# Performance work log

Measured on AMD Instinct MI355X. Metric: run time of the kernel, lower is better.

The kernel has to match this reference:

```python
import jax, jax.numpy as jnp
import numpy as np

N_ITER = 10
N_PRIMAL = 5
N_IONS = 1
B, H, W, A = 1, 96, 96, 60
D = H  # detector bins == H, forced by the reshape in the original code


def _conv(x, w, b):
    y = jax.lax.conv_general_dilated(x, w, (1, 1), [(1, 1), (1, 1)],
                                     dimension_numbers=('NCHW', 'OIHW', 'NCHW'))
    return y + b[None, :, None, None]


def _prelu(x, a):
    return jnp.where(x >= 0, x, a * x)


def _block(x, w1, b1, a1, w2, b2, a2, w3, b3):
    x = _prelu(_conv(x, w1, b1), a1)
    x = _prelu(_conv(x, w2, b2), a2)
    return _conv(x, w3, b3)


def setup_inputs():
    key = jax.random.key(0)
    ks = jax.random.split(key, 12)
    s = 0.05
    dc = 3 * N_IONS      # DualNet input channels
    pc = N_PRIMAL + 1    # PrimalNet input channels
    inp = {
        'dual': jax.random.normal(ks[0], (B, N_IONS, A, D), jnp.float32),
        'primal': jax.random.normal(ks[1], (B, N_PRIMAL, H, W, 1), jnp.float32),
        'g': jax.random.normal(ks[2], (B, N_IONS, A, D), jnp.float32),
        'sysm_angles': jax.random.normal(ks[3], (B, A, H * W, N_IONS * D), jnp.float32) * s,
        'sysm_angles_norm': jax.random.normal(ks[4], (B, A, N_IONS * H, H * W), jnp.float32) * s,
        'dual_w1': jax.random.normal(ks[5], (N_ITER, 32, dc, 3, 3), jnp.float32) * s,
        'dual_b1': jnp.zeros((N_ITER, 32), jnp.float32),
        'dual_a1': jnp.full((N_ITER,), 0.25, jnp.float32),
        'dual_w2': jax.random.normal(ks[6], (N_ITER, 32, 32, 3, 3), jnp.float32) * s,
        'dual_b2': jnp.zeros((N_ITER, 32), jnp.float32),
        'dual_a2': jnp.full((N_ITER,), 0.25, jnp.float32),
        'dual_w3': jax.random.normal(ks[7], (N_ITER, N_IONS, 32, 3, 3), jnp.float32) * s,
        'dual_b3': jnp.zeros((N_ITER, N_IONS), jnp.float32),
        'primal_w1': jax.random.normal(ks[8], (N_ITER, 32, pc, 3, 3), jnp.float32) * s,
        'primal_b1': jnp.zeros((N_ITER, 32), jnp.float32),
        'primal_a1': jnp.full((N_ITER,), 0.25, jnp.float32),
        'primal_w2': jax.random.normal(ks[9], (N_ITER, 32, 32, 3, 3), jnp.float32) * s,
        'primal_b2': jnp.zeros((N_ITER, 32), jnp.float32),
        'primal_a2': jnp.full((N_ITER,), 0.25, jnp.float32),
        'primal_w3': jax.random.normal(ks[10], (N_ITER, N_PRIMAL, 32, 3, 3), jnp.float32) * s,
        'primal_b3': jnp.zeros((N_ITER, N_PRIMAL), jnp.float32),
        'return_all': 0,
    }
    return inp


def _forward(dual, primal, g, sysm_angles, sysm_angles_norm,
             dw1, db1, da1, dw2, db2, da2, dw3, db3,
             pw1, pb1, pa1, pw2, pb2, pa2, pw3, pb3):
    for k in range(N_ITER):
        # forward projection: fortran-flatten primal channel 1 (index h + H*w), batched over all angles
        img_f = primal[:, 1, :, :, 0].transpose(0, 2, 1).reshape(B, H * W)   # [B, H*W]
        prod = jnp.einsum('bamn,bn->bam', sysm_angles_norm, img_f)           # [B, A, N_IONS*H]
        evalop1 = prod.reshape(B, A, H, N_IONS).transpose(0, 3, 1, 2)        # [B, N_IONS, A, D]
        x = jnp.concatenate([dual, evalop1, g], axis=1)
        dual = dual + _block(x, dw1[k], db1[k], da1[k], dw2[k], db2[k], da2[k], dw3[k], db3[k])
        # adjoint (back-projection) summed over angles
        dual2 = dual.transpose(0, 2, 3, 1).reshape(B, A, D * N_IONS)         # [B, A, D*N_IONS]
        vec = jnp.einsum('bavn,ban->bv', sysm_angles, dual2)                 # [B, H*W]
        evalop2 = vec.reshape(B, W, H).transpose(0, 2, 1)[:, None]           # [B, 1, H, W] fortran unflatten
        p2d = primal[..., 0]                                                 # [B, N_PRIMAL, H, W]
        xp = jnp.concatenate([p2d, evalop2], axis=1)
        p2d = p2d + _block(xp, pw1[k], pb1[k], pa1[k], pw2[k], pb2[k], pa2[k], pw3[k], pb3[k])
        primal = p2d[..., None]
    return primal[:, 0:1]  # [B, 1, H, W, 1]


def reference(dual, primal, g, sysm_angles, sysm_angles_norm,
              dual_w1, dual_b1, dual_a1, dual_w2, dual_b2, dual_a2, dual_w3, dual_b3,
              primal_w1, primal_b1, primal_a1, primal_w2, primal_b2, primal_a2, primal_w3, primal_b3,
              return_all):
    return _forward(dual, primal, g, sysm_angles, sysm_angles_norm,
                    dual_w1, dual_b1, dual_a1, dual_w2, dual_b2, dual_a2, dual_w3, dual_b3,
                    primal_w1, primal_b1, primal_a1, primal_w2, primal_b2, primal_a2, primal_w3, primal_b3)
```

## Files before the change

kernel.cpp:

```cpp
#include <hip/hip_runtime.h>

#define AA 60
#define HH 96
#define WW 96
#define DD 96
#define HWP (HH * WW)
#define ADP (AA * DD)
#define NITER 10
#define MATEL (60 * 96 * 9216)

typedef unsigned short ushort8 __attribute__((ext_vector_type(8)));
typedef float float4v __attribute__((ext_vector_type(4)));

__device__ inline float b2f(unsigned short u) {
    return __uint_as_float(((unsigned)u) << 16);
}
__device__ inline unsigned short f2b(float f) {
    unsigned u = __float_as_uint(f);
    u += 0x7FFFu + ((u >> 16) & 1u);
    return (unsigned short)(u >> 16);
}

__global__ __launch_bounds__(256) void cvt_kernel(const float* __restrict__ a,
                                                  const float* __restrict__ b,
                                                  ushort8* __restrict__ da,
                                                  ushort8* __restrict__ db, int n8) {
    int stride = gridDim.x * 256;
    for (int i = blockIdx.x * 256 + threadIdx.x; i < 2 * n8; i += stride) {
        const float* src; ushort8* dst; int j;
        if (i < n8) { src = a; dst = da; j = i; }
        else        { src = b; dst = db; j = i - n8; }
        const float4v* s = reinterpret_cast<const float4v*>(src) + 2 * (size_t)j;
        float4v x = __builtin_nontemporal_load(s);
        float4v y = __builtin_nontemporal_load(s + 1);
        ushort8 o;
        o[0] = f2b(x[0]); o[1] = f2b(x[1]); o[2] = f2b(x[2]); o[3] = f2b(x[3]);
        o[4] = f2b(y[0]); o[5] = f2b(y[1]); o[6] = f2b(y[2]); o[7] = f2b(y[3]);
        dst[j] = o;
    }
}

__global__ __launch_bounds__(256) void init_kernel(const float* __restrict__ dual,
                            const float* __restrict__ g,
                            const float* __restrict__ primal,
                            float* __restrict__ xd, float* __restrict__ xp,
                            float* __restrict__ imgf, float* __restrict__ xp5) {
    int i = blockIdx.x * 256 + threadIdx.x;
    if (i < ADP) { xd[i] = dual[i]; xd[2 * ADP + i] = g[i]; }
    if (i < 5 * HWP) xp[i] = primal[i];
    if (i < HWP) {
        imgf[(i % WW) * HH + i / WW] = primal[HWP + i];
        xp5[i] = 0.f;
    }
}

__global__ __launch_bounds__(256) void einsum1_kernel(const unsigned short* __restrict__ norm,
                               const float* __restrict__ imgf,
                               float* __restrict__ out) {
    int row  = blockIdx.x * 4 + (threadIdx.x >> 6);
    int lane = threadIdx.x & 63;
    const unsigned short* mr = norm + (size_t)row * HWP;
    float s = 0.f;
    for (int k = 0; k < HWP / 512; ++k) {
        int n = 8 * lane + 512 * k;
        ushort8 m8 = *reinterpret_cast<const ushort8*>(mr + n);
        float4 i0 = *reinterpret_cast<const float4*>(imgf + n);
        float4 i1 = *reinterpret_cast<const float4*>(imgf + n + 4);
        s += b2f(m8[0]) * i0.x + b2f(m8[1]) * i0.y + b2f(m8[2]) * i0.z + b2f(m8[3]) * i0.w
           + b2f(m8[4]) * i1.x + b2f(m8[5]) * i1.y + b2f(m8[6]) * i1.z + b2f(m8[7]) * i1.w;
    }
#pragma unroll
    for (int off = 32; off > 0; off >>= 1) s += __shfl_down(s, off);
    if (lane == 0) out[row] = s;
}

__global__ __launch_bounds__(256) void einsum2_kernel(const unsigned short* __restrict__ sysm,
                               const float* __restrict__ xd,
                               float* __restrict__ xp5) {
    __shared__ float sd[4 * DD];
    int t  = threadIdx.x;
    int a0 = (blockIdx.x % 15) * 4;
    int v  = (blockIdx.x / 15) * 256 + t;
    for (int j = t; j < 4 * DD; j += 256) sd[j] = xd[a0 * DD + j];
    __syncthreads();
    float s = 0.f;
    for (int ai = 0; ai < 4; ++ai) {
        const unsigned short* row = sysm + ((size_t)(a0 + ai) * HWP + v) * DD;
        const float* dl = sd + ai * DD;
#pragma unroll
        for (int jj = 0; jj < DD / 8; ++jj) {
            ushort8 m8 = *reinterpret_cast<const ushort8*>(row + 8 * jj);
            s += b2f(m8[0]) * dl[8 * jj]     + b2f(m8[1]) * dl[8 * jj + 1]
               + b2f(m8[2]) * dl[8 * jj + 2] + b2f(m8[3]) * dl[8 * jj + 3]
               + b2f(m8[4]) * dl[8 * jj + 4] + b2f(m8[5]) * dl[8 * jj + 5]
               + b2f(m8[6]) * dl[8 * jj + 6] + b2f(m8[7]) * dl[8 * jj + 7];
        }
    }
    atomicAdd(xp5 + (v % HH) * WW + (v / HH), s);
}

template <int CIN, int NOUT>
__global__ __launch_bounds__(64) void conv_mid(
        const float* __restrict__ in,
        const float* __restrict__ wgt,
        const float* __restrict__ bias,
        const float* __restrict__ alpha,
        float* __restrict__ out,
        int Hc, int Wc) {
    int hw  = Hc * Wc;
    int pix = blockIdx.x * 64 + threadIdx.x;
    int y = pix / Wc, x = pix % Wc;
    int oc0 = blockIdx.y * NOUT;
    const float* wb = wgt + (size_t)oc0 * CIN * 9;
    float a = alpha[0];
    float acc[NOUT];
#pragma unroll
    for (int o = 0; o < NOUT; ++o) acc[o] = bias[oc0 + o];
    for (int ci = 0; ci < CIN; ++ci) {
        const float* ip = in + ci * hw;
#pragma unroll
        for (int ky = 0; ky < 3; ++ky) {
            int yy = y + ky - 1;
            bool yok = (unsigned)yy < (unsigned)Hc;
#pragma unroll
            for (int kx = 0; kx < 3; ++kx) {
                int xx = x + kx - 1;
                bool vok = yok && ((unsigned)xx < (unsigned)Wc);
                float v = ip[vok ? yy * Wc + xx : 0];
                v = vok ? v : 0.f;
#pragma unroll
                for (int o = 0; o < NOUT; ++o)
                    acc[o] += wb[(o * CIN + ci) * 9 + ky * 3 + kx] * v;
            }
        }
    }
#pragma unroll
    for (int o = 0; o < NOUT; ++o) {
        float r = acc[o];
        r = (r >= 0.f) ? r : a * r;
        out[(oc0 + o) * hw + pix] = r;
    }
}

__global__ __launch_bounds__(64) void conv3d_last(const float* __restrict__ in,
        const float* __restrict__ wgt,
        const float* __restrict__ bias,
        float* __restrict__ xd) {
    int pix = blockIdx.x * 64 + threadIdx.x;
    int y = pix / DD, x = pix % DD;
    int c0 = blockIdx.y * 4;
    float r = (blockIdx.y == 0) ? bias[0] : 0.f;
    for (int ci = c0; ci < c0 + 4; ++ci) {
        const float* ip = in + ci * ADP;
#pragma unroll
        for (int ky = 0; ky < 3; ++ky) {
            int yy = y + ky - 1;
            bool yok = (unsigned)yy < (unsigned)AA;
#pragma unroll
            for (int kx = 0; kx < 3; ++kx) {
                int xx = x + kx - 1;
                bool vok = yok && ((unsigned)xx < (unsigned)DD);
                float v = ip[vok ? yy * DD + xx : 0];
                v = vok ? v : 0.f;
                r += wgt[ci * 9 + ky * 3 + kx] * v;
            }
        }
    }
    atomicAdd(xd + pix, r);
}

__global__ __launch_bounds__(64) void conv3p_last(const float* __restrict__ in,
        const float* __restrict__ wgt,
        const float* __restrict__ bias,
        float* __restrict__ xp, float* __restrict__ imgf,
        float* __restrict__ xp5, float* __restrict__ dout, int fin) {
    int pix = blockIdx.x * 64 + threadIdx.x;
    int y = pix / WW, x = pix % WW;
    int oc = blockIdx.y;
    const float* wb = wgt + (size_t)oc * 32 * 9;
    float r = bias[oc];
    for (int ci = 0; ci < 32; ++ci) {
        const float* ip = in + ci * HWP;
#pragma unroll
        for (int ky = 0; ky < 3; ++ky) {
            int yy = y + ky - 1;
            bool yok = (unsigned)yy < (unsigned)HH;
#pragma unroll
            for (int kx = 0; kx < 3; ++kx) {
                int xx = x + kx - 1;
                bool vok = yok && ((unsigned)xx < (unsigned)WW);
                float v = ip[vok ? yy * WW + xx : 0];
                v = vok ? v : 0.f;
                r += wb[ci * 9 + ky * 3 + kx] * v;
            }
        }
    }
    float nv = xp[oc * HWP + pix] + r;
    xp[oc * HWP + pix] = nv;
    if (oc == 1) imgf[x * HH + y] = nv;
    if (oc == 2) xp5[pix] = 0.f;
    if (fin && oc == 0) dout[pix] = nv;
}

extern "C" void kernel_launch(void* const* d_in, const int* in_sizes, int n_in,
                              void* d_out, int out_size, void* d_ws, size_t ws_size,
                              hipStream_t stream) {
    const float* dual   = (const float*)d_in[0];
    const float* primal = (const float*)d_in[1];
    const float* g      = (const float*)d_in[2];
    const float* sysm   = (const float*)d_in[3];
    const float* norm   = (const float*)d_in[4];
    const float* dw1 = (const float*)d_in[5];
    const float* db1 = (const float*)d_in[6];
    const float* da1 = (const float*)d_in[7];
    const float* dw2 = (const float*)d_in[8];
    const float* db2 = (const float*)d_in[9];
    const float* da2 = (const float*)d_in[10];
    const float* dw3 = (const float*)d_in[11];
    const float* db3 = (const float*)d_in[12];
    const float* pw1 = (const float*)d_in[13];
    const float* pb1 = (const float*)d_in[14];
    const float* pa1 = (const float*)d_in[15];
    const float* pw2 = (const float*)d_in[16];
    const float* pb2 = (const float*)d_in[17];
    const float* pa2 = (const float*)d_in[18];
    const float* pw3 = (const float*)d_in[19];
    const float* pb3 = (const float*)d_in[20];

    unsigned short* normb = (unsigned short*)d_ws;
    unsigned short* sysmb = normb + MATEL;
    float* xd   = (float*)(sysmb + MATEL);
    float* xp   = xd + 3 * ADP;
    float* imgf = xp + 6 * HWP;
    float* h1   = imgf + HWP;
    float* h2   = h1 + 32 * ADP;
    float* g1   = h2 + 32 * ADP;
    float* g2   = g1 + 32 * HWP;

    cvt_kernel<<<4096, 256, 0, stream>>>(norm, sysm, (ushort8*)normb, (ushort8*)sysmb, MATEL / 8);
    init_kernel<<<(5 * HWP + 255) / 256, 256, 0, stream>>>(dual, g, primal, xd, xp, imgf, xp + 5 * HWP);

    for (int k = 0; k < NITER; ++k) {
        einsum1_kernel<<<ADP / 4, 256, 0, stream>>>(normb, imgf, xd + ADP);
        conv_mid<3, 2><<<dim3(ADP / 64, 16), 64, 0, stream>>>(
            xd, dw1 + k * 32 * 3 * 9, db1 + k * 32, da1 + k, h1, AA, DD);
        conv_mid<32, 2><<<dim3(ADP / 64, 16), 64, 0, stream>>>(
            h1, dw2 + k * 32 * 32 * 9, db2 + k * 32, da2 + k, h2, AA, DD);
        conv3d_last<<<dim3(ADP / 64, 8), 64, 0, stream>>>(
            h2, dw3 + k * 32 * 9, db3 + k, xd);
        einsum2_kernel<<<15 * 36, 256, 0, stream>>>(sysmb, xd, xp + 5 * HWP);
        conv_mid<6, 2><<<dim3(HWP / 64, 16), 64, 0, stream>>>(
            xp, pw1 + k * 32 * 6 * 9, pb1 + k * 32, pa1 + k, g1, HH, WW);
        conv_mid<32, 2><<<dim3(HWP / 64, 16), 64, 0, stream>>>(
            g1, pw2 + k * 32 * 32 * 9, pb2 + k * 32, pa2 + k, g2, HH, WW);
        conv3p_last<<<dim3(HWP / 64, 5), 64, 0, stream>>>(
            g2, pw3 + k * 5 * 32 * 9, pb3 + k * 5, xp, imgf, xp + 5 * HWP,
            (float*)d_out, k == NITER - 1 ? 1 : 0);
    }
}
```

Baseline: 1.096 ms.

## Split bf16 conversion into flat launches, two rows per wave in einsum1, unroll conv loops

The grid-stride conversion kernel becomes four flat launches, one thread per 8-element chunk, with no loop and no branch on which matrix to convert. einsum1 now has each wave reduce two matrix rows, so each image load is reused twice and the grid is halved. The conv kernels get unroll pragmas on the input-channel loop. This adds launch count and register pressure in return for fewer loop overheads and fewer image reloads.

```diff
diff --git a/kernel.cpp b/kernel.cpp
--- a/kernel.cpp
+++ b/kernel.cpp
@@ -21,23 +21,17 @@
     return (unsigned short)(u >> 16);
 }
 
-__global__ __launch_bounds__(256) void cvt_kernel(const float* __restrict__ a,
-                                                  const float* __restrict__ b,
-                                                  ushort8* __restrict__ da,
-                                                  ushort8* __restrict__ db, int n8) {
-    int stride = gridDim.x * 256;
-    for (int i = blockIdx.x * 256 + threadIdx.x; i < 2 * n8; i += stride) {
-        const float* src; ushort8* dst; int j;
-        if (i < n8) { src = a; dst = da; j = i; }
-        else        { src = b; dst = db; j = i - n8; }
-        const float4v* s = reinterpret_cast<const float4v*>(src) + 2 * (size_t)j;
-        float4v x = __builtin_nontemporal_load(s);
-        float4v y = __builtin_nontemporal_load(s + 1);
-        ushort8 o;
-        o[0] = f2b(x[0]); o[1] = f2b(x[1]); o[2] = f2b(x[2]); o[3] = f2b(x[3]);
-        o[4] = f2b(y[0]); o[5] = f2b(y[1]); o[6] = f2b(y[2]); o[7] = f2b(y[3]);
-        dst[j] = o;
-    }
+__global__ __launch_bounds__(256) void cvtA_kernel(const float* __restrict__ src,
+                                                   ushort8* __restrict__ dst,
+                                                   int base) {
+    int i = base + blockIdx.x * 256 + threadIdx.x;
+    const float4v* s = reinterpret_cast<const float4v*>(src) + 2 * (size_t)i;
+    float4v x = __builtin_nontemporal_load(s);
+    float4v y = __builtin_nontemporal_load(s + 1);
+    ushort8 o;
+    o[0] = f2b(x[0]); o[1] = f2b(x[1]); o[2] = f2b(x[2]); o[3] = f2b(x[3]);
+    o[4] = f2b(y[0]); o[5] = f2b(y[1]); o[6] = f2b(y[2]); o[7] = f2b(y[3]);
+    dst[i] = o;
 }
 
 __global__ __launch_bounds__(256) void init_kernel(const float* __restrict__ dual,
@@ -57,21 +51,28 @@
 __global__ __launch_bounds__(256) void einsum1_kernel(const unsigned short* __restrict__ norm,
                                const float* __restrict__ imgf,
                                float* __restrict__ out) {
-    int row  = blockIdx.x * 4 + (threadIdx.x >> 6);
+    int rp   = blockIdx.x * 4 + (threadIdx.x >> 6);
     int lane = threadIdx.x & 63;
-    const unsigned short* mr = norm + (size_t)row * HWP;
-    float s = 0.f;
+    const unsigned short* r0 = norm + (size_t)(2 * rp) * HWP;
+    const unsigned short* r1 = r0 + HWP;
+    float s0 = 0.f, s1 = 0.f;
     for (int k = 0; k < HWP / 512; ++k) {
         int n = 8 * lane + 512 * k;
-        ushort8 m8 = *reinterpret_cast<const ushort8*>(mr + n);
+        ushort8 a8 = *reinterpret_cast<const ushort8*>(r0 + n);
+        ushort8 b8 = *reinterpret_cast<const ushort8*>(r1 + n);
         float4 i0 = *reinterpret_cast<const float4*>(imgf + n);
         float4 i1 = *reinterpret_cast<const float4*>(imgf + n + 4);
-        s += b2f(m8[0]) * i0.x + b2f(m8[1]) * i0.y + b2f(m8[2]) * i0.z + b2f(m8[3]) * i0.w
-           + b2f(m8[4]) * i1.x + b2f(m8[5]) * i1.y + b2f(m8[6]) * i1.z + b2f(m8[7]) * i1.w;
-    }
-#pragma unroll
-    for (int off = 32; off > 0; off >>= 1) s += __shfl_down(s, off);
-    if (lane == 0) out[row] = s;
+        s0 += b2f(a8[0]) * i0.x + b2f(a8[1]) * i0.y + b2f(a8[2]) * i0.z + b2f(a8[3]) * i0.w
+            + b2f(a8[4]) * i1.x + b2f(a8[5]) * i1.y + b2f(a8[6]) * i1.z + b2f(a8[7]) * i1.w;
+        s1 += b2f(b8[0]) * i0.x + b2f(b8[1]) * i0.y + b2f(b8[2]) * i0.z + b2f(b8[3]) * i0.w
+            + b2f(b8[4]) * i1.x + b2f(b8[5]) * i1.y + b2f(b8[6]) * i1.z + b2f(b8[7]) * i1.w;
+    }
+#pragma unroll
+    for (int off = 32; off > 0; off >>= 1) {
+        s0 += __shfl_down(s0, off);
+        s1 += __shfl_down(s1, off);
+    }
+    if (lane == 0) { out[2 * rp] = s0; out[2 * rp + 1] = s1; }
 }
 
 __global__ __launch_bounds__(256) void einsum2_kernel(const unsigned short* __restrict__ sysm,
@@ -116,6 +117,7 @@
     float acc[NOUT];
 #pragma unroll
     for (int o = 0; o < NOUT; ++o) acc[o] = bias[oc0 + o];
+#pragma unroll 4
     for (int ci = 0; ci < CIN; ++ci) {
         const float* ip = in + ci * hw;
 #pragma unroll
@@ -150,7 +152,9 @@
     int y = pix / DD, x = pix % DD;
     int c0 = blockIdx.y * 4;
     float r = (blockIdx.y == 0) ? bias[0] : 0.f;
-    for (int ci = c0; ci < c0 + 4; ++ci) {
+#pragma unroll
+    for (int cc = 0; cc < 4; ++cc) {
+        int ci = c0 + cc;
         const float* ip = in + ci * ADP;
 #pragma unroll
         for (int ky = 0; ky < 3; ++ky) {
@@ -179,6 +183,7 @@
     int oc = blockIdx.y;
     const float* wb = wgt + (size_t)oc * 32 * 9;
     float r = bias[oc];
+#pragma unroll 4
     for (int ci = 0; ci < 32; ++ci) {
         const float* ip = in + ci * HWP;
 #pragma unroll
@@ -237,11 +242,16 @@
     float* g1   = h2 + 32 * ADP;
     float* g2   = g1 + 32 * HWP;
 
-    cvt_kernel<<<4096, 256, 0, stream>>>(norm, sysm, (ushort8*)normb, (ushort8*)sysmb, MATEL / 8);
+    const int N8 = MATEL / 8;
+    const int HN = N8 / 2;
+    cvtA_kernel<<<HN / 256, 256, 0, stream>>>(norm, (ushort8*)normb, 0);
+    cvtA_kernel<<<HN / 256, 256, 0, stream>>>(norm, (ushort8*)normb, HN);
+    cvtA_kernel<<<HN / 256, 256, 0, stream>>>(sysm, (ushort8*)sysmb, 0);
+    cvtA_kernel<<<HN / 256, 256, 0, stream>>>(sysm, (ushort8*)sysmb, HN);
     init_kernel<<<(5 * HWP + 255) / 256, 256, 0, stream>>>(dual, g, primal, xd, xp, imgf, xp + 5 * HWP);
 
     for (int k = 0; k < NITER; ++k) {
-        einsum1_kernel<<<ADP / 4, 256, 0, stream>>>(normb, imgf, xd + ADP);
+        einsum1_kernel<<<ADP / 8, 256, 0, stream>>>(normb, imgf, xd + ADP);
         conv_mid<3, 2><<<dim3(ADP / 64, 16), 64, 0, stream>>>(
             xd, dw1 + k * 32 * 3 * 9, db1 + k * 32, da1 + k, h1, AA, DD);
         conv_mid<32, 2><<<dim3(ADP / 64, 16), 64, 0, stream>>>(
```

Result: slower. 1.440 ms (+31.4%).
